# Kernel tuning notes

Hardware: AMD Instinct MI355X
Metric: run time of the kernel (lower is better)

## Reference

```python
import jax, jax.numpy as jnp
import numpy as np

B, T, C = 4, 2048, 1024
H, D = 16, 64

def setup_inputs() -> dict:
    key = jax.random.key(0)
    k1, k2, k3 = jax.random.split(key, 3)
    x = jax.random.normal(k1, (B, T, C), dtype=jnp.float32)
    Wqkv = jax.random.normal(k2, (C, 3 * C), dtype=jnp.float32) * (1.0 / np.sqrt(C))
    Wproj = jax.random.normal(k3, (C, C), dtype=jnp.float32) * (1.0 / np.sqrt(C))
    return {"x": x, "Wqkv": Wqkv, "Wproj": Wproj}

def reference(x, Wqkv, Wproj):
    Bx, Tx, Cx = x.shape
    qkv = x @ Wqkv                       # (B, T, 3C)
    q, k, v = jnp.split(qkv, 3, axis=-1)
    # (B, T, C) -> (B, H, T, D)
    q = q.reshape(Bx, Tx, H, D).transpose(0, 2, 1, 3)
    k = k.reshape(Bx, Tx, H, D).transpose(0, 2, 1, 3)
    v = v.reshape(Bx, Tx, H, D).transpose(0, 2, 1, 3)
    att = jnp.einsum('bhqd,bhkd->bhqk', q, k) / jnp.sqrt(jnp.float32(D))
    causal = jnp.tril(jnp.ones((Tx, Tx), dtype=bool))  # (T, T)
    att = jnp.where(causal[None, None, :, :], att, jnp.float32(-jnp.inf))
    att = jax.nn.softmax(att, axis=-1)
    y = jnp.einsum('bhqk,bhkd->bhqd', att, v)          # (B, H, T, D)
    y = y.transpose(0, 2, 1, 3).reshape(Bx, Tx, Cx)
    return y @ Wproj
```

## Files before the change

kernel.cpp:

```cpp
#include <hip/hip_runtime.h>
#include <cstdint>
#include <cstddef>


typedef short bf16x8 __attribute__((ext_vector_type(8)));
typedef float f32x4 __attribute__((ext_vector_type(4)));

#define MFMA32(a, b, c) __builtin_amdgcn_mfma_f32_16x16x32_bf16((a), (b), (c), 0, 0, 0)

__device__ __forceinline__ unsigned short f2b(float f) {
  unsigned int x = __builtin_bit_cast(unsigned int, f);
  x += 0x7fffu + ((x >> 16) & 1u);
  return (unsigned short)(x >> 16);
}

__device__ __forceinline__ unsigned int pack2(float a, float b) {
  return (unsigned int)f2b(a) | ((unsigned int)f2b(b) << 16);
}

__device__ __forceinline__ unsigned int cvtpk(float a, float b) {
  unsigned int r;
  asm("v_cvt_pk_bf16_f32 %0, %1, %2" : "=v"(r) : "v"(a), "v"(b));
  return r;
}

__device__ __forceinline__ float exp2v(float x) {
  float r;
  asm("v_exp_f32 %0, %1" : "=v"(r) : "v"(x));
  return r;
}

__device__ __forceinline__ void gload16(const void* g, void* l) {
  __builtin_amdgcn_global_load_lds(
      (const __attribute__((address_space(1))) void*)g,
      (__attribute__((address_space(3))) void*)l, 16, 0, 0);
}

__global__ __launch_bounds__(256) void k_conv_x(const float* __restrict__ in,
                                                unsigned short* __restrict__ out, int n4) {
  int i = blockIdx.x * 256 + threadIdx.x;
  if (i >= n4) return;
  float4 v = reinterpret_cast<const float4*>(in)[i];
  ushort4 o;
  o.x = f2b(v.x); o.y = f2b(v.y); o.z = f2b(v.z); o.w = f2b(v.w);
  reinterpret_cast<ushort4*>(out)[i] = o;
}

__global__ __launch_bounds__(256) void k_transpose(const float* __restrict__ in,
                                                   unsigned short* __restrict__ out,
                                                   int R, int C) {
  __shared__ float tile[32][33];
  int c0 = blockIdx.x * 32, r0 = blockIdx.y * 32;
  int tx = threadIdx.x & 31, ty = threadIdx.x >> 5;
#pragma unroll
  for (int j = 0; j < 4; ++j)
    tile[ty + 8 * j][tx] = in[(size_t)(r0 + ty + 8 * j) * C + c0 + tx];
  __syncthreads();
#pragma unroll
  for (int j = 0; j < 4; ++j)
    out[(size_t)(c0 + ty + 8 * j) * R + r0 + tx] = f2b(tile[tx][ty + 8 * j]);
}

template <int EPI>
__global__ __launch_bounds__(256) void k_gemm(const unsigned short* __restrict__ A,
                                              const unsigned short* __restrict__ Bt,
                                              float* __restrict__ outF,
                                              unsigned short* __restrict__ q_ws,
                                              unsigned short* __restrict__ k_ws,
                                              unsigned short* __restrict__ v_ws,
                                              int M, int N) {
  constexpr int K = 1024;
  __shared__ unsigned short As[128 * 64];
  __shared__ unsigned short Bs[128 * 64];
  const int bn = blockIdx.x, bm = blockIdx.y;
  const int tid = threadIdx.x;
  const int w = tid >> 6, lane = tid & 63;
  const int wm = w >> 1, wn = w & 1;
  const int c = lane & 15, g = lane >> 4;

  f32x4 acc[4][4];
#pragma unroll
  for (int i = 0; i < 4; ++i)
#pragma unroll
    for (int j = 0; j < 4; ++j) acc[i][j] = (f32x4){0.f, 0.f, 0.f, 0.f};

  const int srow = 32 * w + (lane >> 3);
  const int scol = 8 * (lane & 7);
  const unsigned short* Ag = A + (size_t)(bm * 128 + srow) * K + scol;
  const unsigned short* Bg = Bt + (size_t)(bn * 128 + srow) * K + scol;
  char* AsB = (char*)As + w * 4096;
  char* BsB = (char*)Bs + w * 4096;

  for (int kt = 0; kt < K / 64; ++kt) {
    const int kb = kt * 64;
    __syncthreads();
#pragma unroll
    for (int i = 0; i < 4; ++i) {
      gload16(Ag + (size_t)(8 * i) * K + kb, AsB + i * 1024);
      gload16(Bg + (size_t)(8 * i) * K + kb, BsB + i * 1024);
    }
    asm volatile("s_waitcnt vmcnt(0)" ::: "memory");
    __syncthreads();
#pragma unroll
    for (int u = 0; u < 2; ++u) {
      bf16x8 af[4], bfr[4];
#pragma unroll
      for (int mf = 0; mf < 4; ++mf)
        af[mf] = *(const bf16x8*)((const char*)As + (wm * 64 + mf * 16 + c) * 128 + u * 64 + g * 16);
#pragma unroll
      for (int nf = 0; nf < 4; ++nf)
        bfr[nf] = *(const bf16x8*)((const char*)Bs + (wn * 64 + nf * 16 + c) * 128 + u * 64 + g * 16);
#pragma unroll
      for (int mf = 0; mf < 4; ++mf)
#pragma unroll
        for (int nf = 0; nf < 4; ++nf)
          acc[mf][nf] = MFMA32(af[mf], bfr[nf], acc[mf][nf]);
    }
  }

  const int rowb = bm * 128 + wm * 64;
  const int colb = bn * 128 + wn * 64;
  if (EPI == 1) {
#pragma unroll
    for (int mf = 0; mf < 4; ++mf)
#pragma unroll
      for (int nf = 0; nf < 4; ++nf)
#pragma unroll
        for (int r = 0; r < 4; ++r) {
          int row = rowb + mf * 16 + 4 * g + r;
          int col = colb + nf * 16 + c;
          outF[(size_t)row * N + col] = acc[mf][nf][r];
        }
  } else {
    const float QSC = 0.125f * 1.4426950408889634f;
#pragma unroll
    for (int mf = 0; mf < 4; ++mf)
#pragma unroll
      for (int nf = 0; nf < 4; ++nf)
#pragma unroll
        for (int r = 0; r < 4; ++r) {
          int row = rowb + mf * 16 + 4 * g + r;
          int col = colb + nf * 16 + c;
          int sec = col >> 10, cc = col & 1023;
          int h = cc >> 6, d = cc & 63;
          int b = row >> 11, t = row & 2047;
          float v = acc[mf][nf][r];
          if (sec == 0) {
            q_ws[((size_t)(b * 16 + h) * 2048 + t) * 64 + d] = f2b(v * QSC);
          } else if (sec == 1) {
            int dsw = ((((d >> 3) ^ (t & 7)) & 7) << 3) | (d & 7);
            k_ws[((size_t)(b * 16 + h) * 2048 + t) * 64 + dsw] = f2b(v);
          } else {
            int tsw = (t & ~63) | (((((t >> 3) & 7) ^ (d & 7)) & 7) << 3) | (t & 7);
            v_ws[((size_t)(b * 16 + h) * 64 + d) * 2048 + tsw] = f2b(v);
          }
        }
  }
}

__global__ __launch_bounds__(512) void k_attn(const unsigned short* __restrict__ q_ws,
                                              const unsigned short* __restrict__ k_ws,
                                              const unsigned short* __restrict__ v_ws,
                                              unsigned short* __restrict__ y_ws) {
  constexpr int T = 2048;
  __shared__ unsigned short Ks[2][64 * 64];
  __shared__ unsigned short Vs[2][64 * 64];
  const int f = blockIdx.x;
  const int f2 = (f & 7) * 64 + (f >> 3);
  const int bh = f2 >> 3;
  const int xi = f2 & 7;
  const int tid = threadIdx.x, w = tid >> 6, lane = tid & 63;
  const int c = lane & 15, g = lane >> 4;
  const int cl = c & 7;
  const size_t base = (size_t)bh * T * 64;
  const unsigned short* Kb = k_ws + base;
  const unsigned short* Vb = v_ws + base;
  const unsigned short* Qb = q_ws + base;

  const int srow = w * 8 + (lane >> 3);
  const int sch = lane & 7;

#pragma unroll 1
  for (int ph = 0; ph < 2; ++ph) {
    const int q0 = (ph == 0 ? xi : 15 - xi) * 128;
    const int qrow = q0 + 16 * w + c;
    const int q_max_wave = q0 + 16 * w + 15;
    const int n_kt = (q0 >> 6) + 2;
    bf16x8 qf[2];
#pragma unroll
    for (int u = 0; u < 2; ++u)
      qf[u] = *(const bf16x8*)(Qb + (size_t)qrow * 64 + 32 * u + 8 * g);

    f32x4 yacc[4];
#pragma unroll
    for (int i = 0; i < 4; ++i) yacc[i] = (f32x4){0.f, 0.f, 0.f, 0.f};
    float m_run = -1e30f, l_part = 0.f;

    __syncthreads();
    gload16(Kb + (size_t)srow * 64 + sch * 8, (char*)&Ks[0][0] + w * 1024);
    gload16(Vb + (size_t)srow * T + sch * 8, (char*)&Vs[0][0] + w * 1024);

#pragma unroll 1
    for (int kt = 0; kt < n_kt; ++kt) {
      const int k0 = kt * 64;
      const int cur = kt & 1;
      if (kt + 1 < n_kt) {
        const int k0n = k0 + 64;
        gload16(Kb + (size_t)(k0n + srow) * 64 + sch * 8, (char*)&Ks[cur ^ 1][0] + w * 1024);
        gload16(Vb + (size_t)srow * T + k0n + sch * 8, (char*)&Vs[cur ^ 1][0] + w * 1024);
        asm volatile("s_waitcnt vmcnt(2)" ::: "memory");
      } else {
        asm volatile("s_waitcnt vmcnt(0)" ::: "memory");
      }
      __syncthreads();

      if (k0 <= q_max_wave) {
        const char* KsC = (const char*)&Ks[cur][0];
        const char* VsC = (const char*)&Vs[cur][0];
        f32x4 s[4];
        __builtin_amdgcn_s_setprio(1);
#pragma unroll
        for (int tf = 0; tf < 4; ++tf) {
          bf16x8 kf0 = *(const bf16x8*)(KsC + (16 * tf + c) * 128 + (g ^ cl) * 16);
          bf16x8 kf1 = *(const bf16x8*)(KsC + (16 * tf + c) * 128 + ((4 + g) ^ cl) * 16);
          f32x4 z = (f32x4){0.f, 0.f, 0.f, 0.f};
          z = MFMA32(kf0, qf[0], z);
          s[tf] = MFMA32(kf1, qf[1], z);
        }
        __builtin_amdgcn_s_setprio(0);
        if (k0 + 63 > q0 + 16 * w) {
#pragma unroll
          for (int tf = 0; tf < 4; ++tf)
#pragma unroll
            for (int r = 0; r < 4; ++r)
              if (k0 + 16 * tf + 4 * g + r > qrow) s[tf][r] = -1e30f;
        }
        float mx0 = fmaxf(fmaxf(s[0][0], s[0][1]), fmaxf(s[0][2], s[0][3]));
        float mx1 = fmaxf(fmaxf(s[1][0], s[1][1]), fmaxf(s[1][2], s[1][3]));
        float mx2 = fmaxf(fmaxf(s[2][0], s[2][1]), fmaxf(s[2][2], s[2][3]));
        float mx3 = fmaxf(fmaxf(s[3][0], s[3][1]), fmaxf(s[3][2], s[3][3]));
        float mx = fmaxf(fmaxf(mx0, mx1), fmaxf(mx2, mx3));
        mx = fmaxf(mx, __shfl_xor(mx, 16));
        mx = fmaxf(mx, __shfl_xor(mx, 32));
        if (__any(mx > m_run + 11.5f)) {
          float m_new = fmaxf(m_run, mx);
          float corr = exp2v(m_run - m_new);
          l_part *= corr;
#pragma unroll
          for (int i = 0; i < 4; ++i) yacc[i] *= corr;
          m_run = m_new;
        }
        float p[16];
#pragma unroll
        for (int tf = 0; tf < 4; ++tf)
#pragma unroll
          for (int r = 0; r < 4; ++r) p[tf * 4 + r] = exp2v(s[tf][r] - m_run);
        float ps = ((p[0] + p[1]) + (p[2] + p[3])) + ((p[4] + p[5]) + (p[6] + p[7]));
        ps += ((p[8] + p[9]) + (p[10] + p[11])) + ((p[12] + p[13]) + (p[14] + p[15]));
        l_part += ps;

#pragma unroll
        for (int h = 0; h < 2; ++h) {
          unsigned int lo0 = cvtpk(p[8 * h + 0], p[8 * h + 1]);
          unsigned int hi0 = cvtpk(p[8 * h + 2], p[8 * h + 3]);
          unsigned int lo1 = cvtpk(p[8 * h + 4], p[8 * h + 5]);
          unsigned int hi1 = cvtpk(p[8 * h + 6], p[8 * h + 7]);
          int a2 = 2 * (g & 1);
          int srcA = 16 * a2 + c, srcB = srcA + 16;
          unsigned int Al0 = __shfl(lo0, srcA), Ah0 = __shfl(hi0, srcA);
          unsigned int Al1 = __shfl(lo1, srcA), Ah1 = __shfl(hi1, srcA);
          unsigned int Bl0 = __shfl(lo0, srcB), Bh0 = __shfl(hi0, srcB);
          unsigned int Bl1 = __shfl(lo1, srcB), Bh1 = __shfl(hi1, srcB);
          bool f1 = (g >= 2);
          union { unsigned int u[4]; bf16x8 v; } pf;
          pf.u[0] = f1 ? Al1 : Al0;
          pf.u[1] = f1 ? Ah1 : Ah0;
          pf.u[2] = f1 ? Bl1 : Bl0;
          pf.u[3] = f1 ? Bh1 : Bh0;
          __builtin_amdgcn_s_setprio(1);
#pragma unroll
          for (int df = 0; df < 4; ++df) {
            bf16x8 vf = *(const bf16x8*)(VsC + (16 * df + c) * 128 + ((h * 4 + g) ^ cl) * 16);
            yacc[df] = MFMA32(vf, pf.v, yacc[df]);
          }
          __builtin_amdgcn_s_setprio(0);
        }
      }
      __syncthreads();
    }

    float lt = l_part;
    lt += __shfl_xor(lt, 16);
    lt += __shfl_xor(lt, 32);
    float inv = 1.f / lt;
    const int b = bh >> 4, hh = bh & 15;
#pragma unroll
    for (int df = 0; df < 4; ++df) {
      uint2 o;
      o.x = cvtpk(yacc[df][0] * inv, yacc[df][1] * inv);
      o.y = cvtpk(yacc[df][2] * inv, yacc[df][3] * inv);
      *(uint2*)(y_ws + (size_t)(b * 2048 + qrow) * 1024 + hh * 64 + 16 * df + 4 * g) = o;
    }
  }
}

extern "C" void kernel_launch(void* const* d_in, const int* in_sizes, int n_in,
                              void* d_out, int out_size, void* d_ws, size_t ws_size,
                              hipStream_t stream) {
  const float* x = (const float*)d_in[0];
  const float* Wqkv = (const float*)d_in[1];
  const float* Wproj = (const float*)d_in[2];
  float* out = (float*)d_out;
  char* ws = (char*)d_ws;

  unsigned short* x_bf = (unsigned short*)(ws);
  unsigned short* wqkvT = (unsigned short*)(ws + 16777216);
  unsigned short* wprojT = (unsigned short*)(ws + 23068672);
  unsigned short* q_ws = (unsigned short*)(ws + 25165824);
  unsigned short* k_ws = (unsigned short*)(ws + 41943040);
  unsigned short* v_ws = (unsigned short*)(ws + 58720256);
  unsigned short* y_ws = (unsigned short*)(ws + 75497472);

  k_conv_x<<<8192, 256, 0, stream>>>(x, x_bf, 2097152);
  k_transpose<<<dim3(96, 32), 256, 0, stream>>>(Wqkv, wqkvT, 1024, 3072);
  k_transpose<<<dim3(32, 32), 256, 0, stream>>>(Wproj, wprojT, 1024, 1024);
  k_gemm<0><<<dim3(24, 64), 256, 0, stream>>>(x_bf, wqkvT, nullptr, q_ws, k_ws, v_ws, 8192, 3072);
  k_attn<<<512, 512, 0, stream>>>(q_ws, k_ws, v_ws, y_ws);
  k_gemm<1><<<dim3(8, 64), 256, 0, stream>>>(y_ws, wprojT, out, nullptr, nullptr, nullptr, 8192, 1024);
}
```

Before: 196.5 us.

## Triple-buffer GEMM pipeline with 128x256 tiles, swizzled LDS and XCD-aware block mapping

```diff
diff --git a/kernel.cpp b/kernel.cpp
--- a/kernel.cpp
+++ b/kernel.cpp
@@ -62,20 +62,25 @@
 }
 
 template <int EPI>
-__global__ __launch_bounds__(256) void k_gemm(const unsigned short* __restrict__ A,
+__global__ __launch_bounds__(512) void k_gemm(const unsigned short* __restrict__ A,
                                               const unsigned short* __restrict__ Bt,
                                               float* __restrict__ outF,
                                               unsigned short* __restrict__ q_ws,
                                               unsigned short* __restrict__ k_ws,
                                               unsigned short* __restrict__ v_ws,
                                               int M, int N) {
-  constexpr int K = 1024;
-  __shared__ unsigned short As[128 * 64];
-  __shared__ unsigned short Bs[128 * 64];
-  const int bn = blockIdx.x, bm = blockIdx.y;
-  const int tid = threadIdx.x;
-  const int w = tid >> 6, lane = tid & 63;
-  const int wm = w >> 1, wn = w & 1;
+  constexpr int K = 1024, NKT = 16;
+  __shared__ unsigned short lds[3 * 24576];
+
+  const int nwg = gridDim.x * gridDim.y;
+  const int f = blockIdx.x + blockIdx.y * gridDim.x;
+  const int cpx = nwg >> 3;
+  const int idx = (f & 7) * cpx + (f >> 3);
+  const int bn = idx / gridDim.y;
+  const int bm = idx % gridDim.y;
+
+  const int tid = threadIdx.x, w = tid >> 6, lane = tid & 63;
+  const int wm = w >> 2, wn = w & 3;
   const int c = lane & 15, g = lane >> 4;
 
   f32x4 acc[4][4];
@@ -84,42 +89,73 @@
 #pragma unroll
     for (int j = 0; j < 4; ++j) acc[i][j] = (f32x4){0.f, 0.f, 0.f, 0.f};
 
-  const int srow = 32 * w + (lane >> 3);
-  const int scol = 8 * (lane & 7);
-  const unsigned short* Ag = A + (size_t)(bm * 128 + srow) * K + scol;
-  const unsigned short* Bg = Bt + (size_t)(bn * 128 + srow) * K + scol;
-  char* AsB = (char*)As + w * 4096;
-  char* BsB = (char*)Bs + w * 4096;
-
-  for (int kt = 0; kt < K / 64; ++kt) {
-    const int kb = kt * 64;
-    __syncthreads();
-#pragma unroll
-    for (int i = 0; i < 4; ++i) {
-      gload16(Ag + (size_t)(8 * i) * K + kb, AsB + i * 1024);
-      gload16(Bg + (size_t)(8 * i) * K + kb, BsB + i * 1024);
-    }
-    asm volatile("s_waitcnt vmcnt(0)" ::: "memory");
-    __syncthreads();
-#pragma unroll
-    for (int u = 0; u < 2; ++u) {
+  const int srow = w * 16 + (lane >> 2);
+  const int scs = (((lane & 3) ^ ((lane >> 3) & 3))) * 8;
+  const unsigned short* Ag = A + (size_t)(bm * 128 + srow) * K + scs;
+  const unsigned short* Bg = Bt + (size_t)(bn * 256 + srow) * K + scs;
+
+#define STAGE(kt, h, bi)                                                       \
+  {                                                                            \
+    const int kb = (kt) * 64 + (h) * 32;                                       \
+    gload16(Ag + kb, &lds[(bi) * 24576 + (h) * 4096 + w * 512]);               \
+    gload16(Bg + kb, &lds[(bi) * 24576 + 8192 + (h) * 8192 + w * 512]);        \
+    gload16(Bg + (size_t)128 * K + kb,                                         \
+            &lds[(bi) * 24576 + 8192 + (h) * 8192 + 4096 + w * 512]);          \
+  }
+
+  const int rsw = (g ^ ((c >> 1) & 3)) * 8;
+  const int arow = (wm * 64 + c) * 32 + rsw;
+  const int brow = (wn * 64 + c) * 32 + rsw;
+
+  STAGE(0, 0, 0)
+  STAGE(0, 1, 0)
+  STAGE(1, 0, 1)
+  STAGE(1, 1, 1)
+  asm volatile("s_waitcnt vmcnt(9)" ::: "memory");
+  __builtin_amdgcn_s_barrier();
+
+  int b0 = 0;
+#pragma unroll 1
+  for (int kt = 0; kt < NKT; ++kt) {
+    int b2 = b0 + 2;
+    if (b2 >= 3) b2 -= 3;
+    const unsigned short* Ab = &lds[b0 * 24576];
+    const unsigned short* Bb = &lds[b0 * 24576 + 8192];
+#pragma unroll
+    for (int kk = 0; kk < 2; ++kk) {
       bf16x8 af[4], bfr[4];
 #pragma unroll
       for (int mf = 0; mf < 4; ++mf)
-        af[mf] = *(const bf16x8*)((const char*)As + (wm * 64 + mf * 16 + c) * 128 + u * 64 + g * 16);
+        af[mf] = *(const bf16x8*)(Ab + kk * 4096 + arow + mf * 512);
 #pragma unroll
       for (int nf = 0; nf < 4; ++nf)
-        bfr[nf] = *(const bf16x8*)((const char*)Bs + (wn * 64 + nf * 16 + c) * 128 + u * 64 + g * 16);
+        bfr[nf] = *(const bf16x8*)(Bb + kk * 8192 + brow + nf * 512);
+      if (kt + 2 < NKT) STAGE(kt + 2, kk, b2)
+      if (kt + 2 < NKT) {
+        asm volatile("s_waitcnt vmcnt(9)" ::: "memory");
+      } else if (kt == NKT - 2) {
+        if (kk == 0) asm volatile("s_waitcnt vmcnt(6)" ::: "memory");
+        else         asm volatile("s_waitcnt vmcnt(3)" ::: "memory");
+      } else {
+        asm volatile("s_waitcnt vmcnt(0)" ::: "memory");
+      }
+      __builtin_amdgcn_s_barrier();
+      __builtin_amdgcn_s_setprio(1);
 #pragma unroll
       for (int mf = 0; mf < 4; ++mf)
 #pragma unroll
         for (int nf = 0; nf < 4; ++nf)
           acc[mf][nf] = MFMA32(af[mf], bfr[nf], acc[mf][nf]);
+      __builtin_amdgcn_s_setprio(0);
+      __builtin_amdgcn_s_barrier();
     }
+    ++b0;
+    if (b0 == 3) b0 = 0;
   }
+#undef STAGE
 
   const int rowb = bm * 128 + wm * 64;
-  const int colb = bn * 128 + wn * 64;
+  const int colb = bn * 256 + wn * 64;
   if (EPI == 1) {
 #pragma unroll
     for (int mf = 0; mf < 4; ++mf)
@@ -212,7 +248,7 @@
       } else {
         asm volatile("s_waitcnt vmcnt(0)" ::: "memory");
       }
-      __syncthreads();
+      __builtin_amdgcn_s_barrier();
 
       if (k0 <= q_max_wave) {
         const char* KsC = (const char*)&Ks[cur][0];
@@ -286,7 +322,7 @@
           __builtin_amdgcn_s_setprio(0);
         }
       }
-      __syncthreads();
+      __builtin_amdgcn_s_barrier();
     }
 
     float lt = l_part;
@@ -324,7 +360,7 @@
   k_conv_x<<<8192, 256, 0, stream>>>(x, x_bf, 2097152);
   k_transpose<<<dim3(96, 32), 256, 0, stream>>>(Wqkv, wqkvT, 1024, 3072);
   k_transpose<<<dim3(32, 32), 256, 0, stream>>>(Wproj, wprojT, 1024, 1024);
-  k_gemm<0><<<dim3(24, 64), 256, 0, stream>>>(x_bf, wqkvT, nullptr, q_ws, k_ws, v_ws, 8192, 3072);
+  k_gemm<0><<<dim3(12, 64), 512, 0, stream>>>(x_bf, wqkvT, nullptr, q_ws, k_ws, v_ws, 8192, 3072);
   k_attn<<<512, 512, 0, stream>>>(q_ws, k_ws, v_ws, y_ws);
-  k_gemm<1><<<dim3(8, 64), 256, 0, stream>>>(y_ws, wprojT, out, nullptr, nullptr, nullptr, 8192, 1024);
-}
+  k_gemm<1><<<dim3(4, 64), 512, 0, stream>>>(y_ws, wprojT, out, nullptr, nullptr, nullptr, 8192, 1024);
+}
```

After: 201.3 us. 1.02x slower.

## Rewrite GEMM as 256x256 tile, 8-wave kernel with double-buffered staged loads

Applied to the files above, without the earlier changes.

```diff
diff --git a/kernel.cpp b/kernel.cpp
--- a/kernel.cpp
+++ b/kernel.cpp
@@ -62,7 +62,7 @@
 }
 
 template <int EPI>
-__global__ __launch_bounds__(256) void k_gemm(const unsigned short* __restrict__ A,
+__global__ __launch_bounds__(512) void k_gemm(const unsigned short* __restrict__ A,
                                               const unsigned short* __restrict__ Bt,
                                               float* __restrict__ outF,
                                               unsigned short* __restrict__ q_ws,
@@ -70,59 +70,123 @@
                                               unsigned short* __restrict__ v_ws,
                                               int M, int N) {
   constexpr int K = 1024;
-  __shared__ unsigned short As[128 * 64];
-  __shared__ unsigned short Bs[128 * 64];
-  const int bn = blockIdx.x, bm = blockIdx.y;
-  const int tid = threadIdx.x;
-  const int w = tid >> 6, lane = tid & 63;
-  const int wm = w >> 1, wn = w & 1;
+  __shared__ unsigned short lds[65536];
+
+  const int nbn = gridDim.x;
+  const int nwg = gridDim.x * gridDim.y;
+  const int f = blockIdx.x + blockIdx.y * gridDim.x;
+  const int cpx = nwg >> 3;
+  const int idx = (f & 7) * cpx + (f >> 3);
+  const int bm = idx / nbn, bn = idx % nbn;
+
+  const int tid = threadIdx.x, w = tid >> 6, lane = tid & 63;
+  const int wm = w >> 2, wn = w & 3;
   const int c = lane & 15, g = lane >> 4;
-
-  f32x4 acc[4][4];
-#pragma unroll
-  for (int i = 0; i < 4; ++i)
+  const int cl8 = c & 7;
+  const int ch0 = g ^ cl8, ch1 = ch0 ^ 4;
+
+  const unsigned short* Ag = A + (size_t)(bm * 256) * K;
+  const unsigned short* Bg = Bt + (size_t)(bn * 256) * K;
+  const int r0 = w * 8 + (lane >> 3);
+  const int sch = (lane & 7) ^ (lane >> 3);
+
+  f32x4 acc[8][4];
+#pragma unroll
+  for (int i = 0; i < 8; ++i)
 #pragma unroll
     for (int j = 0; j < 4; ++j) acc[i][j] = (f32x4){0.f, 0.f, 0.f, 0.f};
 
-  const int srow = 32 * w + (lane >> 3);
-  const int scol = 8 * (lane & 7);
-  const unsigned short* Ag = A + (size_t)(bm * 128 + srow) * K + scol;
-  const unsigned short* Bg = Bt + (size_t)(bn * 128 + srow) * K + scol;
-  char* AsB = (char*)As + w * 4096;
-  char* BsB = (char*)Bs + w * 4096;
-
-  for (int kt = 0; kt < K / 64; ++kt) {
-    const int kb = kt * 64;
-    __syncthreads();
-#pragma unroll
-    for (int i = 0; i < 4; ++i) {
-      gload16(Ag + (size_t)(8 * i) * K + kb, AsB + i * 1024);
-      gload16(Bg + (size_t)(8 * i) * K + kb, BsB + i * 1024);
-    }
-    asm volatile("s_waitcnt vmcnt(0)" ::: "memory");
-    __syncthreads();
-#pragma unroll
-    for (int u = 0; u < 2; ++u) {
-      bf16x8 af[4], bfr[4];
-#pragma unroll
-      for (int mf = 0; mf < 4; ++mf)
-        af[mf] = *(const bf16x8*)((const char*)As + (wm * 64 + mf * 16 + c) * 128 + u * 64 + g * 16);
-#pragma unroll
-      for (int nf = 0; nf < 4; ++nf)
-        bfr[nf] = *(const bf16x8*)((const char*)Bs + (wn * 64 + nf * 16 + c) * 128 + u * 64 + g * 16);
-#pragma unroll
-      for (int mf = 0; mf < 4; ++mf)
-#pragma unroll
-        for (int nf = 0; nf < 4; ++nf)
-          acc[mf][nf] = MFMA32(af[mf], bfr[nf], acc[mf][nf]);
-    }
-  }
-
-  const int rowb = bm * 128 + wm * 64;
-  const int colb = bn * 128 + wn * 64;
+  bf16x8 af[2][2], bfr[4][2];
+  const int sA0 = wm, sA1 = 4 + wm;
+  const int sB0 = 2 + (wn >> 1), sB1 = 6 + (wn >> 1);
+
+#define LDA2(sA, mf0)                                                          \
+  {                                                                            \
+    _Pragma("unroll") for (int mi = 0; mi < 2; ++mi) {                         \
+      const int rb = (sA) * 8192 + ((mf0) + mi) * 1024 + c * 64;               \
+      af[mi][0] = *(const bf16x8*)&lds[rb + ch0 * 8];                          \
+      af[mi][1] = *(const bf16x8*)&lds[rb + ch1 * 8];                          \
+    }                                                                          \
+  }
+#define LDB(sB)                                                                \
+  {                                                                            \
+    _Pragma("unroll") for (int nf = 0; nf < 4; ++nf) {                         \
+      const int rb = (sB) * 8192 + ((wn & 1) * 64 + nf * 16 + c) * 64;         \
+      bfr[nf][0] = *(const bf16x8*)&lds[rb + ch0 * 8];                         \
+      bfr[nf][1] = *(const bf16x8*)&lds[rb + ch1 * 8];                         \
+    }                                                                          \
+  }
+#define MM2(mf0)                                                               \
+  {                                                                            \
+    _Pragma("unroll") for (int mi = 0; mi < 2; ++mi)                           \
+        _Pragma("unroll") for (int nf = 0; nf < 4; ++nf) {                     \
+      acc[(mf0) + mi][nf] = MFMA32(af[mi][0], bfr[nf][0], acc[(mf0) + mi][nf]);\
+      acc[(mf0) + mi][nf] = MFMA32(af[mi][1], bfr[nf][1], acc[(mf0) + mi][nf]);\
+    }                                                                          \
+  }
+#define STG_A(t, h)                                                            \
+  {                                                                            \
+    gload16(Ag + (size_t)((h) * 128 + r0) * K + (t) * 64 + sch * 8,            \
+            &lds[(((t) & 1) * 4 + (h)) * 8192 + w * 512]);                     \
+    gload16(Ag + (size_t)((h) * 128 + 64 + r0) * K + (t) * 64 + sch * 8,       \
+            &lds[(((t) & 1) * 4 + (h)) * 8192 + 4096 + w * 512]);              \
+  }
+#define STG_B(t, h)                                                            \
+  {                                                                            \
+    gload16(Bg + (size_t)((h) * 128 + r0) * K + (t) * 64 + sch * 8,            \
+            &lds[(((t) & 1) * 4 + 2 + (h)) * 8192 + w * 512]);                 \
+    gload16(Bg + (size_t)((h) * 128 + 64 + r0) * K + (t) * 64 + sch * 8,       \
+            &lds[(((t) & 1) * 4 + 2 + (h)) * 8192 + 4096 + w * 512]);          \
+  }
+#define BAR                                                                    \
+  __builtin_amdgcn_s_barrier();                                                \
+  __builtin_amdgcn_sched_barrier(0)
+#define LGKM0 asm volatile("s_waitcnt lgkmcnt(0)" ::: "memory")
+#define VMC4 asm volatile("s_waitcnt vmcnt(4)" ::: "memory")
+#define VMC0 asm volatile("s_waitcnt vmcnt(0)" ::: "memory")
+#define PR1 __builtin_amdgcn_s_setprio(1)
+#define PR0 __builtin_amdgcn_s_setprio(0)
+
+  STG_A(0, 0) STG_A(0, 1) STG_B(0, 0) STG_B(0, 1) STG_B(1, 0) STG_B(1, 1)
+  VMC4;
+  BAR;
+
+#pragma unroll 1
+  for (int it = 0; it < 8; ++it) {
+    const int t0 = 2 * it, t1 = t0 + 1;
+    const bool st = (it < 7);
+    LDB(sB0) LDA2(sA0, 0) STG_A(t1, 0)
+    BAR; LGKM0; PR1; MM2(0) PR0; BAR;
+    LDA2(sA0, 2) STG_A(t1, 1)
+    BAR; LGKM0; PR1; MM2(2) PR0; BAR;
+    LDA2(sA0, 4) if (st) STG_B(t0 + 2, 0)
+    BAR; LGKM0; PR1; MM2(4) PR0; BAR;
+    LDA2(sA0, 6) if (st) STG_B(t0 + 2, 1)
+    BAR; LGKM0; PR1; MM2(6) PR0;
+    if (st) { VMC4; } else { VMC0; }
+    BAR;
+    LDB(sB1) LDA2(sA1, 0) if (st) STG_A(t0 + 2, 0)
+    BAR; LGKM0; PR1; MM2(0) PR0; BAR;
+    LDA2(sA1, 2) if (st) STG_A(t0 + 2, 1)
+    BAR; LGKM0; PR1; MM2(2) PR0; BAR;
+    LDA2(sA1, 4) if (st) STG_B(t1 + 2, 0)
+    BAR; LGKM0; PR1; MM2(4) PR0; BAR;
+    LDA2(sA1, 6) if (st) STG_B(t1 + 2, 1)
+    BAR; LGKM0; PR1; MM2(6) PR0;
+    if (st) { VMC4; }
+    BAR;
+  }
+#undef LDA2
+#undef LDB
+#undef MM2
+#undef STG_A
+#undef STG_B
+
+  const int rowb = bm * 256 + wm * 128;
+  const int colb = bn * 256 + wn * 64;
   if (EPI == 1) {
 #pragma unroll
-    for (int mf = 0; mf < 4; ++mf)
+    for (int mf = 0; mf < 8; ++mf)
 #pragma unroll
       for (int nf = 0; nf < 4; ++nf)
 #pragma unroll
@@ -134,7 +198,7 @@
   } else {
     const float QSC = 0.125f * 1.4426950408889634f;
 #pragma unroll
-    for (int mf = 0; mf < 4; ++mf)
+    for (int mf = 0; mf < 8; ++mf)
 #pragma unroll
       for (int nf = 0; nf < 4; ++nf)
 #pragma unroll
@@ -212,7 +276,7 @@
       } else {
         asm volatile("s_waitcnt vmcnt(0)" ::: "memory");
       }
-      __syncthreads();
+      __builtin_amdgcn_s_barrier();
 
       if (k0 <= q_max_wave) {
         const char* KsC = (const char*)&Ks[cur][0];
@@ -286,7 +350,7 @@
           __builtin_amdgcn_s_setprio(0);
         }
       }
-      __syncthreads();
+      __builtin_amdgcn_s_barrier();
     }
 
     float lt = l_part;
@@ -324,7 +388,7 @@
   k_conv_x<<<8192, 256, 0, stream>>>(x, x_bf, 2097152);
   k_transpose<<<dim3(96, 32), 256, 0, stream>>>(Wqkv, wqkvT, 1024, 3072);
   k_transpose<<<dim3(32, 32), 256, 0, stream>>>(Wproj, wprojT, 1024, 1024);
-  k_gemm<0><<<dim3(24, 64), 256, 0, stream>>>(x_bf, wqkvT, nullptr, q_ws, k_ws, v_ws, 8192, 3072);
+  k_gemm<0><<<dim3(12, 32), 512, 0, stream>>>(x_bf, wqkvT, nullptr, q_ws, k_ws, v_ws, 8192, 3072);
   k_attn<<<512, 512, 0, stream>>>(q_ws, k_ws, v_ws, y_ws);
-  k_gemm<1><<<dim3(8, 64), 256, 0, stream>>>(y_ws, wprojT, out, nullptr, nullptr, nullptr, 8192, 1024);
-}
+  k_gemm<1><<<dim3(4, 32), 512, 0, stream>>>(y_ws, wprojT, out, nullptr, nullptr, nullptr, 8192, 1024);
+}
```

New measurement: 196.6 us. No clear change (+0.0%).
